# Optimization experiments

Measured on AMD Instinct MI355X. Metric: run time of the kernel, lower is better.

## Reference

```python
import jax, jax.numpy as jnp
import numpy as np

KEY_DIM, VALUE_DIM, NUM_HEAD, OUT_DIM = 128, 64, 4, 64
HEAD_KDIM = KEY_DIM // NUM_HEAD   # 32
HEAD_VDIM = VALUE_DIM // NUM_HEAD # 16

def _xavier(key, shape):
    # xavier_uniform over (fan_in=shape[0], fan_out=prod(shape[1:])) like torch
    fan_in, fan_out = shape[0], int(np.prod(shape[1:]))
    lim = float(np.sqrt(6.0 / (fan_in + fan_out)))
    return jax.random.uniform(key, shape, jnp.float32, -lim, lim)

def setup_inputs() -> dict:
    key = jax.random.key(0)
    ks = jax.random.split(key, 7)
    B, Q, K = 2, 4096, 4096
    return {
        "q_data": jax.random.normal(ks[0], (B, Q, KEY_DIM), jnp.float32),
        "m_data": jax.random.normal(ks[1], (B, K, VALUE_DIM), jnp.float32),
        "mask": jax.random.randint(ks[2], (B, K), 0, 2, jnp.int32),
        "q_weights": _xavier(ks[3], (KEY_DIM, NUM_HEAD, HEAD_KDIM)),
        "k_weights": _xavier(ks[4], (VALUE_DIM, NUM_HEAD, HEAD_KDIM)),
        "v_weights": _xavier(ks[5], (VALUE_DIM, NUM_HEAD, HEAD_VDIM)),
        "o_weights": _xavier(ks[6], (NUM_HEAD, HEAD_VDIM, OUT_DIM)),
        "o_bias": jnp.zeros((OUT_DIM,), jnp.float32),
    }

def reference(q_data, m_data, mask, q_weights, k_weights, v_weights, o_weights, o_bias):
    head_kdim = q_weights.shape[-1]
    scale = head_kdim ** (-0.5)
    Q = jnp.einsum('bqa,ahc->bqhc', q_data, q_weights) * scale
    K = jnp.einsum('bka,ahc->bkhc', m_data, k_weights)
    V = jnp.einsum('bka,ahc->bkhc', m_data, v_weights)
    logits = jnp.einsum('bqhc,bkhc->bhqk', Q, K)
    neg = jnp.finfo(logits.dtype).min
    logits = jnp.where(mask[:, None, None, :] == 0, neg, logits)
    weights = jax.nn.softmax(logits, axis=-1)
    weight_avg = jnp.einsum('bhqk,bkhc->bqhc', weights, V)
    return jnp.einsum('bqhc,hco->bqo', weight_avg, o_weights) + o_bias
```

## Files before the change

kernel.cpp:

```cpp
#include <hip/hip_runtime.h>
#include <stdint.h>

#define B_  2
#define QN  4096
#define KN  4096
#define AD  128
#define MD  64
#define H_  4
#define C_  32
#define CV  16
#define OD  64

typedef short bf16x8 __attribute__((ext_vector_type(8)));
typedef short bf16x4 __attribute__((ext_vector_type(4)));
typedef float f32x4  __attribute__((ext_vector_type(4)));

__device__ __forceinline__ short f2bf(float f) {
  union { float f; unsigned u; } v; v.f = f;
  unsigned r = v.u + 0x7fffu + ((v.u >> 16) & 1u);
  return (short)(r >> 16);
}
__device__ __forceinline__ unsigned pack2t(float a, float b) {
  union { float f; unsigned u; } ua, ub; ua.f = a; ub.f = b;
  return __builtin_amdgcn_perm(ub.u, ua.u, 0x07060302u);
}
__device__ __forceinline__ bf16x4 pack4t(f32x4 p) {
  union { unsigned u[2]; bf16x4 v; } t;
  t.u[0] = pack2t(p[0], p[1]); t.u[1] = pack2t(p[2], p[3]);
  return t.v;
}
__device__ __forceinline__ bf16x8 cvt8(f32x4 a, f32x4 b) {
  bf16x8 o;
  o[0]=f2bf(a[0]); o[1]=f2bf(a[1]); o[2]=f2bf(a[2]); o[3]=f2bf(a[3]);
  o[4]=f2bf(b[0]); o[5]=f2bf(b[1]); o[6]=f2bf(b[2]); o[7]=f2bf(b[3]);
  return o;
}

__global__ __launch_bounds__(256) void k_compact(const int* __restrict__ mask,
                                                 int* __restrict__ idx, int* __restrict__ kc) {
  __shared__ int wcnt[64];
  __shared__ int wbase[64];
  const int b = blockIdx.x;
  const int lane = threadIdx.x & 63, wid = threadIdx.x >> 6;
  unsigned long long bals[16];
  #pragma unroll
  for (int p = 0; p < 16; ++p) {
    const int seg = wid*16 + p;
    const int m = mask[b*KN + seg*64 + lane] != 0;
    bals[p] = __ballot(m);
    if (lane == 0) wcnt[seg] = __popcll(bals[p]);
  }
  __syncthreads();
  if (wid == 0) {
    int v = wcnt[lane]; int incl = v;
    for (int d = 1; d < 64; d <<= 1) { int o = __shfl_up(incl, d); if (lane >= d) incl += o; }
    wbase[lane] = incl - v;
    if (lane == 63) kc[b] = incl;
  }
  __syncthreads();
  #pragma unroll
  for (int p = 0; p < 16; ++p) {
    const int seg = wid*16 + p;
    if ((bals[p] >> lane) & 1ull) {
      const int pos = __popcll(bals[p] & ((1ull << lane) - 1ull));
      idx[b*KN + wbase[seg] + pos] = seg*64 + lane;
    }
  }
}

__global__ __launch_bounds__(256) void k_proj(const float* __restrict__ qdf, const float* __restrict__ mdf,
                                              const float* __restrict__ qwf, const float* __restrict__ kwf,
                                              const float* __restrict__ vwf,
                                              const int* __restrict__ idx, const int* __restrict__ kc,
                                              short* __restrict__ Qp, short* __restrict__ Kp,
                                              short* __restrict__ Vpt) {
  const int lane = threadIdx.x & 63;
  const int n = lane & 15, quad = lane >> 4;
  const f32x4 z4 = {0.f,0.f,0.f,0.f};
  if (blockIdx.x < 1024) {
    const int t = blockIdx.x*4 + (threadIdx.x >> 6);
    const int rt = t >> 3, ct = t & 7;
    const int row = rt*16 + n;
    const int hc0 = ct*16;
    f32x4 acc = z4;
    #pragma unroll
    for (int ak = 0; ak < 4; ++ak) {
      const int a0 = ak*32 + quad*8;
      const float* ap = qdf + row*AD + a0;
      bf16x8 afrag = cvt8(*(const f32x4*)ap, *(const f32x4*)(ap + 4));
      bf16x8 bfrag;
      #pragma unroll
      for (int j = 0; j < 8; ++j) bfrag[j] = f2bf(qwf[(a0 + j)*128 + hc0 + n]);
      acc = __builtin_amdgcn_mfma_f32_16x16x32_bf16(afrag, bfrag, acc, 0, 0, 0);
    }
    const int h = hc0 >> 5, c0 = (hc0 & 31) + n;
    const float s = 0.17677669529663687f * 1.44269504088896341f;
    #pragma unroll
    for (int r = 0; r < 4; ++r) {
      const int rr = rt*16 + quad*4 + r;
      const int bb = rr >> 12, q = rr & 4095;
      Qp[((bb*H_ + h)*QN + q)*C_ + c0] = f2bf(acc[r] * s);
    }
    return;
  }
  const int t = (blockIdx.x - 1024)*4 + (threadIdx.x >> 6);
  const int b = t / 3072; const int rem = t - b*3072;
  const int rt = rem / 12, ct = rem - rt*12;
  const int Kc = kc[b];
  const int nch = (Kc + 31) >> 5;
  if (rt*16 >= nch*32) return;
  const int j = rt*16 + n;
  const int valid = (j < Kc);
  const int src = valid ? idx[b*KN + j] : 0;
  const float* mrow = mdf + (b*KN + src)*MD;
  const int hc = ct*16 + n;
  f32x4 acc = z4;
  #pragma unroll
  for (int ch = 0; ch < 2; ++ch) {
    const int a0 = ch*32 + quad*8;
    bf16x8 afrag = cvt8(*(const f32x4*)(mrow + a0), *(const f32x4*)(mrow + a0 + 4));
    if (!valid) {
      #pragma unroll
      for (int jj = 0; jj < 8; ++jj) afrag[jj] = 0;
    }
    bf16x8 bfrag;
    if (ct < 8) {
      #pragma unroll
      for (int jj = 0; jj < 8; ++jj) bfrag[jj] = f2bf(kwf[(a0 + jj)*128 + hc]);
    } else {
      #pragma unroll
      for (int jj = 0; jj < 8; ++jj) bfrag[jj] = f2bf(vwf[(a0 + jj)*64 + hc - 128]);
    }
    acc = __builtin_amdgcn_mfma_f32_16x16x32_bf16(afrag, bfrag, acc, 0, 0, 0);
  }
  if (ct < 8) {
    const int h = hc >> 5, c = hc & 31;
    #pragma unroll
    for (int r = 0; r < 4; ++r) {
      const int jj2 = rt*16 + quad*4 + r;
      Kp[((b*H_ + h)*KN + jj2)*C_ + c] = f2bf(acc[r]);
    }
  } else {
    const int hc2 = hc - 128; const int h = hc2 >> 4, cv = hc2 & 15;
    bf16x4 pk; pk[0]=f2bf(acc[0]); pk[1]=f2bf(acc[1]); pk[2]=f2bf(acc[2]); pk[3]=f2bf(acc[3]);
    *(bf16x4*)(Vpt + ((b*H_ + h)*CV + cv)*KN + rt*16 + quad*4) = pk;
  }
}

__global__ __launch_bounds__(512) void k_attn(const short* __restrict__ Qp, const short* __restrict__ Kp,
                                              const short* __restrict__ Vpt, const int* __restrict__ kc,
                                              const float* __restrict__ w2f, const float* __restrict__ obf,
                                              float* __restrict__ out) {
  __shared__ short P_lds[8][32*40];
  __shared__ float Of[2][32*65];
  __shared__ float Lb[2*4*32];
  __shared__ short ObfA[32*72];
  const int lane = threadIdx.x & 63, wid = threadIdx.x >> 6;
  const int h = wid & 3, split = wid >> 2;
  const int flatq = blockIdx.x * 32;
  const int b = flatq >> 12, qt = flatq & 4095;
  const int bh = b*H_ + h;
  const int n = lane & 15, quad = lane >> 4;
  const short* Qb = Qp + (bh*QN + qt)*C_;
  const short* Kb = Kp + bh*KN*C_;
  const short* Vb = Vpt + bh*CV*KN;
  const bf16x8 qb0 = *(const bf16x8*)(Qb + n*C_ + quad*8);
  const bf16x8 qb1 = *(const bf16x8*)(Qb + (16 + n)*C_ + quad*8);
  const int Kc = kc[b];
  const int nch = (Kc + 31) >> 5;
  const f32x4 z4 = {0.f,0.f,0.f,0.f};
  f32x4 o0 = z4, o1 = z4;
  float l0 = 0.f, l1 = 0.f;
  short* Pw = &P_lds[wid][0];
  bf16x8 kf0, kf1, va;
  int ci = split;
  if (ci < nch) {
    const int kb = ci*32;
    kf0 = *(const bf16x8*)(Kb + (kb + n)*C_ + quad*8);
    kf1 = *(const bf16x8*)(Kb + (kb + 16 + n)*C_ + quad*8);
    va  = *(const bf16x8*)(Vb + n*KN + kb + quad*8);
  }
  for (; ci < nch; ci += 2) {
    const bf16x8 ckf0 = kf0, ckf1 = kf1, cva = va;
    const int cin = ci + 2;
    if (cin < nch) {
      const int kb2 = cin*32;
      kf0 = *(const bf16x8*)(Kb + (kb2 + n)*C_ + quad*8);
      kf1 = *(const bf16x8*)(Kb + (kb2 + 16 + n)*C_ + quad*8);
      va  = *(const bf16x8*)(Vb + n*KN + kb2 + quad*8);
    }
    f32x4 s00 = __builtin_amdgcn_mfma_f32_16x16x32_bf16(ckf0, qb0, z4, 0, 0, 0);
    f32x4 s01 = __builtin_amdgcn_mfma_f32_16x16x32_bf16(ckf0, qb1, z4, 0, 0, 0);
    f32x4 s10 = __builtin_amdgcn_mfma_f32_16x16x32_bf16(ckf1, qb0, z4, 0, 0, 0);
    f32x4 s11 = __builtin_amdgcn_mfma_f32_16x16x32_bf16(ckf1, qb1, z4, 0, 0, 0);
    f32x4 p00, p01, p10, p11;
    #pragma unroll
    for (int r = 0; r < 4; ++r) {
      p00[r] = __builtin_amdgcn_exp2f(s00[r]);
      p01[r] = __builtin_amdgcn_exp2f(s01[r]);
      p10[r] = __builtin_amdgcn_exp2f(s10[r]);
      p11[r] = __builtin_amdgcn_exp2f(s11[r]);
    }
    l0 += ((p00[0]+p00[1])+(p00[2]+p00[3])) + ((p10[0]+p10[1])+(p10[2]+p10[3]));
    l1 += ((p01[0]+p01[1])+(p01[2]+p01[3])) + ((p11[0]+p11[1])+(p11[2]+p11[3]));
    *(bf16x4*)(Pw + n*40 + quad*4)           = pack4t(p00);
    *(bf16x4*)(Pw + n*40 + 16 + quad*4)      = pack4t(p10);
    *(bf16x4*)(Pw + (16+n)*40 + quad*4)      = pack4t(p01);
    *(bf16x4*)(Pw + (16+n)*40 + 16 + quad*4) = pack4t(p11);
    const bf16x8 pb0 = *(const bf16x8*)(Pw + n*40 + quad*8);
    const bf16x8 pb1 = *(const bf16x8*)(Pw + (16+n)*40 + quad*8);
    o0 = __builtin_amdgcn_mfma_f32_16x16x32_bf16(cva, pb0, o0, 0, 0, 0);
    o1 = __builtin_amdgcn_mfma_f32_16x16x32_bf16(cva, pb1, o1, 0, 0, 0);
  }
  #pragma unroll
  for (int r = 0; r < 4; ++r) {
    const int hc = h*16 + quad*4 + r;
    Of[split][n*65 + hc]      = o0[r];
    Of[split][(16+n)*65 + hc] = o1[r];
  }
  l0 += __shfl_xor(l0, 16); l0 += __shfl_xor(l0, 32);
  l1 += __shfl_xor(l1, 16); l1 += __shfl_xor(l1, 32);
  if (lane < 16) {
    Lb[split*128 + h*32 + lane]      = l0;
    Lb[split*128 + h*32 + 16 + lane] = l1;
  }
  __syncthreads();
  {
    const float npad = (float)(nch*32 - Kc);
    const int e = threadIdx.x * 4;
    const int q = e >> 6, hc = e & 63;
    const int hh = hc >> 4;
    const float l = Lb[hh*32 + q] + Lb[128 + hh*32 + q] - npad;
    const float inv = 1.00135f / l;
    bf16x4 pk;
    #pragma unroll
    for (int jj = 0; jj < 4; ++jj)
      pk[jj] = f2bf((Of[0][q*65 + hc + jj] + Of[1][q*65 + hc + jj]) * inv);
    *(bf16x4*)(ObfA + q*72 + hc) = pk;
  }
  __syncthreads();
  {
    const int mt = wid & 1, nt = wid >> 1;
    f32x4 acc = z4;
    #pragma unroll
    for (int kchunk = 0; kchunk < 2; ++kchunk) {
      const bf16x8 afrag = *(const bf16x8*)(ObfA + (mt*16 + n)*72 + kchunk*32 + quad*8);
      bf16x8 bfrag;
      #pragma unroll
      for (int jj = 0; jj < 8; ++jj)
        bfrag[jj] = f2bf(w2f[(kchunk*32 + quad*8 + jj)*64 + nt*16 + n]);
      acc = __builtin_amdgcn_mfma_f32_16x16x32_bf16(afrag, bfrag, acc, 0, 0, 0);
    }
    const int ocol = nt*16 + n;
    const float bias = obf[ocol];
    #pragma unroll
    for (int r = 0; r < 4; ++r) {
      const int qg = flatq + mt*16 + quad*4 + r;
      out[qg*64 + ocol] = acc[r] + bias;
    }
  }
}

extern "C" void kernel_launch(void* const* d_in, const int* in_sizes, int n_in,
                              void* d_out, int out_size, void* d_ws, size_t ws_size,
                              hipStream_t stream) {
  const float* qd  = (const float*)d_in[0];
  const float* md  = (const float*)d_in[1];
  const int*   msk = (const int*)  d_in[2];
  const float* qw  = (const float*)d_in[3];
  const float* kw  = (const float*)d_in[4];
  const float* vw  = (const float*)d_in[5];
  const float* ow  = (const float*)d_in[6];
  const float* ob  = (const float*)d_in[7];
  float* out = (float*)d_out;

  char* ws = (char*)d_ws;
  int*   idx = (int*)  (ws);
  int*   kc  = (int*)  (ws + (32<<10));
  short* Qp  = (short*)(ws + (64<<10));
  short* Kp  = (short*)(ws + (64<<10) + (2u<<20));
  short* Vpt = (short*)(ws + (64<<10) + (4u<<20));

  hipLaunchKernelGGL(k_compact, dim3(2),    dim3(256), 0, stream, msk, idx, kc);
  hipLaunchKernelGGL(k_proj,    dim3(2560), dim3(256), 0, stream, qd, md, qw, kw, vw, idx, kc, Qp, Kp, Vpt);
  hipLaunchKernelGGL(k_attn,    dim3(256),  dim3(512), 0, stream, Qp, Kp, Vpt, kc, ow, ob, out);
}
```

Before: 108.2 us.

## Fuse mask compaction into projection kernel and double attention key-split waves

Removes the separate mask-compaction kernel. Each K/V projection block now recomputes the ballot masks and prefix sums in shared memory, and finds each row's source index by binary search over prefix counts and bit popcounts. This saves one launch and its serialization, at the cost of redundant mask reads and scans in every block. The attention kernel moves from 512 to 1024 threads, splitting the key chunks four ways instead of two, with one shared-memory pool reused across phases. That gives more waves per block to hide latency, but adds reduction work and a longer critical path per block.

Result: faster. 103.2 us (-4.7%).

```diff
diff --git a/kernel.cpp b/kernel.cpp
--- a/kernel.cpp
+++ b/kernel.cpp
@@ -36,49 +36,18 @@
   return o;
 }
 
-__global__ __launch_bounds__(256) void k_compact(const int* __restrict__ mask,
-                                                 int* __restrict__ idx, int* __restrict__ kc) {
-  __shared__ int wcnt[64];
-  __shared__ int wbase[64];
-  const int b = blockIdx.x;
-  const int lane = threadIdx.x & 63, wid = threadIdx.x >> 6;
-  unsigned long long bals[16];
-  #pragma unroll
-  for (int p = 0; p < 16; ++p) {
-    const int seg = wid*16 + p;
-    const int m = mask[b*KN + seg*64 + lane] != 0;
-    bals[p] = __ballot(m);
-    if (lane == 0) wcnt[seg] = __popcll(bals[p]);
-  }
-  __syncthreads();
-  if (wid == 0) {
-    int v = wcnt[lane]; int incl = v;
-    for (int d = 1; d < 64; d <<= 1) { int o = __shfl_up(incl, d); if (lane >= d) incl += o; }
-    wbase[lane] = incl - v;
-    if (lane == 63) kc[b] = incl;
-  }
-  __syncthreads();
-  #pragma unroll
-  for (int p = 0; p < 16; ++p) {
-    const int seg = wid*16 + p;
-    if ((bals[p] >> lane) & 1ull) {
-      const int pos = __popcll(bals[p] & ((1ull << lane) - 1ull));
-      idx[b*KN + wbase[seg] + pos] = seg*64 + lane;
-    }
-  }
-}
-
 __global__ __launch_bounds__(256) void k_proj(const float* __restrict__ qdf, const float* __restrict__ mdf,
                                               const float* __restrict__ qwf, const float* __restrict__ kwf,
                                               const float* __restrict__ vwf,
-                                              const int* __restrict__ idx, const int* __restrict__ kc,
+                                              const int* __restrict__ mask, int* __restrict__ kc,
                                               short* __restrict__ Qp, short* __restrict__ Kp,
                                               short* __restrict__ Vpt) {
   const int lane = threadIdx.x & 63;
+  const int wid = threadIdx.x >> 6;
   const int n = lane & 15, quad = lane >> 4;
   const f32x4 z4 = {0.f,0.f,0.f,0.f};
   if (blockIdx.x < 1024) {
-    const int t = blockIdx.x*4 + (threadIdx.x >> 6);
+    const int t = blockIdx.x*4 + wid;
     const int rt = t >> 3, ct = t & 7;
     const int row = rt*16 + n;
     const int hc0 = ct*16;
@@ -103,15 +72,50 @@
     }
     return;
   }
-  const int t = (blockIdx.x - 1024)*4 + (threadIdx.x >> 6);
-  const int b = t / 3072; const int rem = t - b*3072;
+  __shared__ unsigned long long balS[64];
+  __shared__ int pref[64];
+  __shared__ int kcS;
+  const int bidx = blockIdx.x - 1024;
+  const int b = (bidx*4) / 3072;
+  #pragma unroll
+  for (int p = 0; p < 16; ++p) {
+    const int seg = wid*16 + p;
+    const unsigned long long bal = __ballot(mask[b*KN + seg*64 + lane] != 0);
+    if (lane == 0) balS[seg] = bal;
+  }
+  __syncthreads();
+  if (wid == 0) {
+    int v = __popcll(balS[lane]); int incl = v;
+    for (int d = 1; d < 64; d <<= 1) { int o = __shfl_up(incl, d); if (lane >= d) incl += o; }
+    pref[lane] = incl - v;
+    if (lane == 63) kcS = incl;
+  }
+  __syncthreads();
+  const int Kc = kcS;
+  const int nch = (Kc + 31) >> 5;
+  const int t = bidx*4 + wid;
+  const int rem = t - b*3072;
   const int rt = rem / 12, ct = rem - rt*12;
-  const int Kc = kc[b];
-  const int nch = (Kc + 31) >> 5;
+  if (rem == 0 && lane == 0) kc[b] = Kc;
   if (rt*16 >= nch*32) return;
   const int j = rt*16 + n;
   const int valid = (j < Kc);
-  const int src = valid ? idx[b*KN + j] : 0;
+  int src = 0;
+  if (valid) {
+    int seg = 0;
+    #pragma unroll
+    for (int st = 32; st >= 1; st >>= 1)
+      if (seg + st < 64 && pref[seg + st] <= j) seg += st;
+    int r2 = j - pref[seg];
+    unsigned long long m = balS[seg];
+    int pos = 0;
+    #pragma unroll
+    for (int w = 32; w >= 1; w >>= 1) {
+      const int c = __popcll(m & ((1ull << w) - 1ull));
+      if (r2 >= c) { r2 -= c; m >>= w; pos += w; }
+    }
+    src = seg*64 + pos;
+  }
   const float* mrow = mdf + (b*KN + src)*MD;
   const int hc = ct*16 + n;
   f32x4 acc = z4;
@@ -147,14 +151,11 @@
   }
 }
 
-__global__ __launch_bounds__(512) void k_attn(const short* __restrict__ Qp, const short* __restrict__ Kp,
-                                              const short* __restrict__ Vpt, const int* __restrict__ kc,
-                                              const float* __restrict__ w2f, const float* __restrict__ obf,
-                                              float* __restrict__ out) {
-  __shared__ short P_lds[8][32*40];
-  __shared__ float Of[2][32*65];
-  __shared__ float Lb[2*4*32];
-  __shared__ short ObfA[32*72];
+__global__ __launch_bounds__(1024) void k_attn(const short* __restrict__ Qp, const short* __restrict__ Kp,
+                                               const short* __restrict__ Vpt, const int* __restrict__ kc,
+                                               const float* __restrict__ w2f, const float* __restrict__ obf,
+                                               float* __restrict__ out) {
+  __shared__ __attribute__((aligned(16))) char pool[40960];
   const int lane = threadIdx.x & 63, wid = threadIdx.x >> 6;
   const int h = wid & 3, split = wid >> 2;
   const int flatq = blockIdx.x * 32;
@@ -171,7 +172,7 @@
   const f32x4 z4 = {0.f,0.f,0.f,0.f};
   f32x4 o0 = z4, o1 = z4;
   float l0 = 0.f, l1 = 0.f;
-  short* Pw = &P_lds[wid][0];
+  short* Pw = (short*)(pool + wid*2560);
   bf16x8 kf0, kf1, va;
   int ci = split;
   if (ci < nch) {
@@ -180,9 +181,9 @@
     kf1 = *(const bf16x8*)(Kb + (kb + 16 + n)*C_ + quad*8);
     va  = *(const bf16x8*)(Vb + n*KN + kb + quad*8);
   }
-  for (; ci < nch; ci += 2) {
+  for (; ci < nch; ci += 4) {
     const bf16x8 ckf0 = kf0, ckf1 = kf1, cva = va;
-    const int cin = ci + 2;
+    const int cin = ci + 4;
     if (cin < nch) {
       const int kb2 = cin*32;
       kf0 = *(const bf16x8*)(Kb + (kb2 + n)*C_ + quad*8);
@@ -212,11 +213,15 @@
     o0 = __builtin_amdgcn_mfma_f32_16x16x32_bf16(cva, pb0, o0, 0, 0, 0);
     o1 = __builtin_amdgcn_mfma_f32_16x16x32_bf16(cva, pb1, o1, 0, 0, 0);
   }
+  __syncthreads();
+  float* Of   = (float*)pool;
+  float* Lb   = (float*)(pool + 33280);
+  short* ObfA = (short*)(pool + 35328);
   #pragma unroll
   for (int r = 0; r < 4; ++r) {
     const int hc = h*16 + quad*4 + r;
-    Of[split][n*65 + hc]      = o0[r];
-    Of[split][(16+n)*65 + hc] = o1[r];
+    Of[split*2080 + n*65 + hc]        = o0[r];
+    Of[split*2080 + (16+n)*65 + hc]   = o1[r];
   }
   l0 += __shfl_xor(l0, 16); l0 += __shfl_xor(l0, 32);
   l1 += __shfl_xor(l1, 16); l1 += __shfl_xor(l1, 32);
@@ -227,19 +232,22 @@
   __syncthreads();
   {
     const float npad = (float)(nch*32 - Kc);
-    const int e = threadIdx.x * 4;
+    const int e = threadIdx.x * 2;
     const int q = e >> 6, hc = e & 63;
     const int hh = hc >> 4;
-    const float l = Lb[hh*32 + q] + Lb[128 + hh*32 + q] - npad;
+    const float l = (Lb[hh*32 + q] + Lb[128 + hh*32 + q])
+                  + (Lb[256 + hh*32 + q] + Lb[384 + hh*32 + q]) - npad;
     const float inv = 1.00135f / l;
-    bf16x4 pk;
-    #pragma unroll
-    for (int jj = 0; jj < 4; ++jj)
-      pk[jj] = f2bf((Of[0][q*65 + hc + jj] + Of[1][q*65 + hc + jj]) * inv);
-    *(bf16x4*)(ObfA + q*72 + hc) = pk;
-  }
-  __syncthreads();
-  {
+    const float v0 = ((Of[q*65 + hc]     + Of[2080 + q*65 + hc])
+                    + (Of[4160 + q*65 + hc] + Of[6240 + q*65 + hc])) * inv;
+    const float v1 = ((Of[q*65 + hc + 1] + Of[2080 + q*65 + hc + 1])
+                    + (Of[4160 + q*65 + hc + 1] + Of[6240 + q*65 + hc + 1])) * inv;
+    union { unsigned u; short s[2]; } pk;
+    pk.s[0] = f2bf(v0); pk.s[1] = f2bf(v1);
+    *(unsigned*)(ObfA + q*72 + hc) = pk.u;
+  }
+  __syncthreads();
+  if (wid < 8) {
     const int mt = wid & 1, nt = wid >> 1;
     f32x4 acc = z4;
     #pragma unroll
@@ -275,13 +283,11 @@
   float* out = (float*)d_out;
 
   char* ws = (char*)d_ws;
-  int*   idx = (int*)  (ws);
-  int*   kc  = (int*)  (ws + (32<<10));
+  int*   kc  = (int*)  (ws);
   short* Qp  = (short*)(ws + (64<<10));
   short* Kp  = (short*)(ws + (64<<10) + (2u<<20));
   short* Vpt = (short*)(ws + (64<<10) + (4u<<20));
 
-  hipLaunchKernelGGL(k_compact, dim3(2),    dim3(256), 0, stream, msk, idx, kc);
-  hipLaunchKernelGGL(k_proj,    dim3(2560), dim3(256), 0, stream, qd, md, qw, kw, vw, idx, kc, Qp, Kp, Vpt);
-  hipLaunchKernelGGL(k_attn,    dim3(256),  dim3(512), 0, stream, Qp, Kp, Vpt, kc, ow, ob, out);
-}
+  hipLaunchKernelGGL(k_proj, dim3(2560), dim3(256),  0, stream, qd, md, qw, kw, vw, msk, kc, Qp, Kp, Vpt);
+  hipLaunchKernelGGL(k_attn, dim3(256),  dim3(1024), 0, stream, Qp, Kp, Vpt, kc, ow, ob, out);
+}
```
